# Optimization experiments

Hardware: AMD Instinct MI355X
Metric: run time of the kernel (lower is better)

## Reference

```python
import jax, jax.numpy as jnp
import numpy as np

B, S, D, H = 2, 2048, 1024, 16
HD = D // H  # head_dim = 64


def setup_inputs() -> dict:
    key = jax.random.key(0)
    k1, k2, k3 = jax.random.split(key, 3)
    x = jax.random.normal(k1, (B, S, D), dtype=jnp.float32)
    W_qkv = jax.random.normal(k2, (D, 3 * D), dtype=jnp.float32) * (D ** -0.5)
    b_qkv = jnp.zeros((3 * D,), dtype=jnp.float32)
    W_proj = jax.random.normal(k3, (D, D), dtype=jnp.float32) * (D ** -0.5)
    b_proj = jnp.zeros((D,), dtype=jnp.float32)
    return {"x": x, "W_qkv": W_qkv, "b_qkv": b_qkv, "W_proj": W_proj, "b_proj": b_proj}


def reference(x, W_qkv, b_qkv, W_proj, b_proj):
    b, s, d = x.shape
    scale = HD ** -0.5
    qkv = x @ W_qkv + b_qkv                       # [B,S,3D]
    q, k, v = jnp.split(qkv, 3, axis=-1)
    # [B,S,D] -> [B,H,S,HD]
    def to_heads(t):
        return t.reshape(b, s, H, HD).transpose(0, 2, 1, 3)
    q, k, v = map(to_heads, (q, k, v))
    scores = jnp.einsum('bhqd,bhkd->bhqk', q, k) * scale  # [B,H,S,S]
    causal = jnp.triu(jnp.ones((s, s), dtype=bool), k=1)
    scores = jnp.where(causal[None, None], -jnp.inf, scores)
    attn = jax.nn.softmax(scores, axis=-1)
    out = jnp.einsum('bhqk,bhkd->bhqd', attn, v)  # [B,H,S,HD]
    out = out.transpose(0, 2, 1, 3).reshape(b, s, d)
    return out @ W_proj + b_proj
```

## Files before the change

### kernel.cpp

```cpp
#include <hip/hip_runtime.h>

using frag_t = __attribute__((ext_vector_type(8))) short;
using f32x4  = __attribute__((ext_vector_type(4))) float;

#define L2E 1.4426950408889634f

#if __has_builtin(__builtin_amdgcn_exp2f)
#define EXP2(x) __builtin_amdgcn_exp2f(x)
#else
#define EXP2(x) exp2f(x)
#endif

constexpr int B_  = 2, S_ = 2048, D_ = 1024, H_ = 16, HD_ = 64;
constexpr int M_  = B_ * S_;
constexpr float QSCALE = 0.125f * L2E;

__device__ __forceinline__ ushort f2bf(float f) {
  union { float f; unsigned u; } v; v.f = f;
  unsigned u = v.u;
  unsigned r = (u + 0x7FFFu + ((u >> 16) & 1u)) >> 16;
  return (ushort)r;
}

__device__ __forceinline__ void gld_lds16(const ushort* g, ushort* l) {
  __builtin_amdgcn_global_load_lds((const __attribute__((address_space(1))) void*)g,
                                   (__attribute__((address_space(3))) void*)l, 16, 0, 0);
}

__global__ __launch_bounds__(256) void k_prep(
    const float* __restrict__ x, const float* __restrict__ Wqkv,
    const float* __restrict__ Wproj,
    ushort* __restrict__ Xbf, ushort* __restrict__ Wqt, ushort* __restrict__ Wpt) {
  int blk = blockIdx.x, tid = threadIdx.x;
  if (blk < 1024) {
    size_t base = (size_t)blk * 4096 + tid * 4;
    #pragma unroll
    for (int i = 0; i < 4; ++i) {
      float4 f = *(const float4*)(x + base + i * 1024);
      ushort4 o;
      o.x = f2bf(f.x); o.y = f2bf(f.y); o.z = f2bf(f.z); o.w = f2bf(f.w);
      *(ushort4*)(Xbf + base + i * 1024) = o;
    }
  } else {
    __shared__ float tile[64][65];
    const float* in; ushort* out; int N, K, bx, by;
    if (blk < 1024 + 768) { int b2 = blk - 1024; in = Wqkv;  out = Wqt; N = 3072; K = 1024; bx = b2 % 48; by = b2 / 48; }
    else                  { int b2 = blk - 1792; in = Wproj; out = Wpt; N = 1024; K = 1024; bx = b2 % 16; by = b2 / 16; }
    int n0 = bx * 64, k0 = by * 64;
    int tx = tid & 63, ty = tid >> 6;
    #pragma unroll
    for (int i = 0; i < 16; ++i)
      tile[ty + i * 4][tx] = in[(size_t)(k0 + ty + i * 4) * N + n0 + tx];
    __syncthreads();
    #pragma unroll
    for (int i = 0; i < 16; ++i)
      out[(size_t)(n0 + ty + i * 4) * K + k0 + tx] = f2bf(tile[tx][ty + i * 4]);
  }
}

__global__ __launch_bounds__(512, 2) void k_gemm8(
    const ushort* __restrict__ A, const ushort* __restrict__ Bt,
    const float* __restrict__ bias,
    ushort* __restrict__ Qo, ushort* __restrict__ Ko, ushort* __restrict__ Vo) {
  __shared__ ushort smem[65536];
  int tid = threadIdx.x;
  int lane = tid & 63, wave = tid >> 6;
  int quad = lane >> 4, li = lane & 15;
  int wm = wave >> 2, wn = wave & 3;
  int wg = blockIdx.x;
  int swz = (wg & 7) * 24 + (wg >> 3);
  int by = swz / 12, bx = swz % 12;
  int m0 = by * 256, n0 = bx * 256;
  const ushort* Asrc = A  + (size_t)m0 * 1024;
  const ushort* Bsrc = Bt + (size_t)n0 * 1024;
  int srow   = lane >> 2;
  int schunk = (lane & 3) ^ ((lane >> 4) & 3);
  int pos    = (quad ^ ((li >> 2) & 3)) * 8;

#define STG(BI, ISB, KS, KT) do { \
    const ushort* _s = (ISB) ? Bsrc : Asrc; \
    ushort* _d = &smem[((BI)*4 + (ISB)*2 + (KS)) * 8192]; \
    _Pragma("unroll") \
    for (int j = 0; j < 2; ++j) \
      gld_lds16(&_s[(size_t)(j*128 + wave*16 + srow) * 1024 + (KT)*64 + (KS)*32 + schunk*8], \
                &_d[(j*128 + wave*16) * 32]); \
  } while (0)

  f32x4 acc[8][4] = {};
  frag_t af[8], bf[2];

#define PH(BI, KS, NH, STGS, W4) do { \
    if ((NH) == 0) { \
      _Pragma("unroll") \
      for (int mi = 0; mi < 8; ++mi) \
        af[mi] = *(const frag_t*)&smem[((BI)*4 + (KS)) * 8192 + (wm*128 + mi*16 + li) * 32 + pos]; \
    } \
    _Pragma("unroll") \
    for (int nj = 0; nj < 2; ++nj) \
      bf[nj] = *(const frag_t*)&smem[((BI)*4 + 2 + (KS)) * 8192 + (wn*64 + ((NH)*2 + nj)*16 + li) * 32 + pos]; \
    STGS; \
    if (W4) asm volatile("s_waitcnt vmcnt(4)" ::: "memory"); \
    asm volatile("s_barrier" ::: "memory"); \
    __builtin_amdgcn_s_setprio(1); \
    _Pragma("unroll") \
    for (int mi = 0; mi < 8; ++mi) { \
      acc[mi][(NH)*2+0] = __builtin_amdgcn_mfma_f32_16x16x32_bf16(af[mi], bf[0], acc[mi][(NH)*2+0], 0, 0, 0); \
      acc[mi][(NH)*2+1] = __builtin_amdgcn_mfma_f32_16x16x32_bf16(af[mi], bf[1], acc[mi][(NH)*2+1], 0, 0, 0); \
    } \
    __builtin_amdgcn_s_setprio(0); \
    asm volatile("s_barrier" ::: "memory"); \
  } while (0)

  STG(0,0,0,0); STG(0,1,0,0); STG(0,0,1,0); STG(0,1,1,0);
  STG(1,0,0,1); STG(1,1,0,1);
  asm volatile("s_waitcnt vmcnt(4)" ::: "memory");
  asm volatile("s_barrier" ::: "memory");

  for (int it = 0; it < 8; ++it) {
    int t1 = 2*it + 1;
    int t2 = (2*it + 2 < 16) ? 2*it + 2 : 15;
    int t3 = (2*it + 3 < 16) ? 2*it + 3 : 15;
    PH(0,0,0, STG(1,0,1,t1), 0);
    PH(0,0,1, STG(1,1,1,t1), 0);
    PH(0,1,0, STG(0,0,0,t2), 0);
    PH(0,1,1, STG(0,1,0,t2), 1);
    PH(1,0,0, STG(0,0,1,t2), 0);
    PH(1,0,1, STG(0,1,1,t2), 0);
    PH(1,1,0, STG(1,0,0,t3), 0);
    PH(1,1,1, STG(1,1,0,t3), 1);
  }
#undef PH
#undef STG

  asm volatile("s_waitcnt vmcnt(0)" ::: "memory");
  __syncthreads();

  int which = (n0 + wn * 64) >> 10;
  if (which < 2) {
    #pragma unroll
    for (int ni = 0; ni < 4; ++ni) {
      int gcol = n0 + wn * 64 + ni * 16 + li;
      float bv = bias[gcol];
      int d = gcol & 1023, h = d >> 6, hd = d & 63;
      #pragma unroll
      for (int mi = 0; mi < 8; ++mi)
        #pragma unroll
        for (int r = 0; r < 4; ++r) {
          int grow = m0 + wm * 128 + mi * 16 + quad * 4 + r;
          int b = grow >> 11, s = grow & 2047;
          size_t off = (((size_t)b * H_ + h) * S_ + s) * HD_ + hd;
          float v = acc[mi][ni][r] + bv;
          if (which == 0) Qo[off] = f2bf(v * QSCALE);
          else            Ko[off] = f2bf(v);
        }
    }
  } else {
    ushort* vl = &smem[wave * 8192];
    #pragma unroll
    for (int ni = 0; ni < 4; ++ni) {
      int row = ni * 16 + li;
      float bv = bias[n0 + wn * 64 + row];
      int rx = (row & 7) << 3;
      #pragma unroll
      for (int mi = 0; mi < 8; ++mi) {
        int g  = (mi & 1) * 4 + quad;
        int gm = g & 3;
        int gp = (gm == 1 || gm == 2) ? (g ^ 3) : g;
        #pragma unroll
        for (int r = 0; r < 4; ++r) {
          int col = (mi >> 1) * 32 + gp * 4 + r;
          vl[row * 128 + (col ^ rx)] = f2bf(acc[mi][ni][r] + bv);
        }
      }
    }
    int h  = ((n0 & 1023) + wn * 64) >> 6;
    int b  = m0 >> 11;
    int s0 = (m0 & 2047) + wm * 128;
    size_t vbase = ((size_t)b * H_ + h) * HD_ * S_;
    #pragma unroll
    for (int i = 0; i < 16; ++i) {
      int row = i * 4 + quad;
      int col = li * 8;
      *(uint4*)&Vo[vbase + (size_t)row * S_ + s0 + col] =
          *(const uint4*)&vl[row * 128 + (col ^ ((row & 7) << 3))];
    }
  }
}

__global__ __launch_bounds__(256) void k_proj(
    const ushort* __restrict__ A, const ushort* __restrict__ Bt,
    const float* __restrict__ bias, float* __restrict__ Co) {
  constexpr int BM = 128, BN = 64, BK = 64, MI = 4, NI = 2;
  constexpr int N = 1024, K = 1024;
  __shared__ ushort smem[(BM + BN) * BK];
  ushort* As = smem;
  ushort* Bs = smem + BM * BK;
  int tid  = threadIdx.x;
  int lane = tid & 63, wave = tid >> 6;
  int quad = lane >> 4, li = lane & 15;
  int mbase = (wave >> 1) * (MI * 16);
  int nbase = (wave & 1) * 32;
  int m0 = blockIdx.y * BM, n0 = blockIdx.x * BN;
  int srow = lane >> 3;
  int scol = ((lane & 7) ^ srow) * 8;
  f32x4 acc[MI][NI] = {};
  for (int k0 = 0; k0 < K; k0 += BK) {
    #pragma unroll
    for (int i = 0; i < 4; ++i) {
      int rbase = i * 32 + wave * 8;
      gld_lds16(&A[(size_t)(m0 + rbase + srow) * K + k0 + scol], &As[rbase * BK]);
    }
    #pragma unroll
    for (int i = 0; i < 2; ++i) {
      int rbase = wave * 16 + i * 8;
      gld_lds16(&Bt[(size_t)(n0 + rbase + srow) * K + k0 + scol], &Bs[rbase * BK]);
    }
    __syncthreads();
    #pragma unroll
    for (int ks = 0; ks < 2; ++ks) {
      frag_t af[MI], bf[NI];
      #pragma unroll
      for (int mi = 0; mi < MI; ++mi)
        af[mi] = *(const frag_t*)&As[(mbase + mi * 16 + li) * BK + (((ks * 4 + quad) ^ (li & 7)) * 8)];
      #pragma unroll
      for (int ni = 0; ni < NI; ++ni)
        bf[ni] = *(const frag_t*)&Bs[(nbase + ni * 16 + li) * BK + (((ks * 4 + quad) ^ (li & 7)) * 8)];
      #pragma unroll
      for (int mi = 0; mi < MI; ++mi)
        #pragma unroll
        for (int ni = 0; ni < NI; ++ni)
          acc[mi][ni] = __builtin_amdgcn_mfma_f32_16x16x32_bf16(af[mi], bf[ni], acc[mi][ni], 0, 0, 0);
    }
    __syncthreads();
  }
  #pragma unroll
  for (int mi = 0; mi < MI; ++mi)
    #pragma unroll
    for (int ni = 0; ni < NI; ++ni) {
      int gcol = n0 + nbase + ni * 16 + li;
      float bv = bias[gcol];
      #pragma unroll
      for (int r = 0; r < 4; ++r) {
        int grow = m0 + mbase + mi * 16 + quad * 4 + r;
        Co[(size_t)grow * N + gcol] = acc[mi][ni][r] + bv;
      }
    }
}

__global__ __launch_bounds__(256) void k_attn(
    const ushort* __restrict__ Q, const ushort* __restrict__ K,
    const ushort* __restrict__ Vt, ushort* __restrict__ O) {
  __shared__ ushort Kbuf[2][64 * 64];
  __shared__ ushort Vbuf[2][64 * 64];
  int lane = threadIdx.x & 63, wave = threadIdx.x >> 6;
  int quad = lane >> 4, li = lane & 15;
  int bh = blockIdx.x;
  int yi = (int)blockIdx.y;
  int qb = (yi < 8) ? 31 - yi : (yi < 16) ? yi - 8 : (yi < 24) ? 39 - yi : yi - 16;
  int b = bh >> 4, hh = bh & 15;
  int q0 = qb * 64 + wave * 16;
  const ushort* Qb = Q  + (size_t)bh * S_ * HD_;
  const ushort* Kb = K  + (size_t)bh * S_ * HD_;
  const ushort* Vb = Vt + (size_t)bh * HD_ * S_;

  frag_t qf[2];
  #pragma unroll
  for (int ks = 0; ks < 2; ++ks)
    qf[ks] = *(const frag_t*)&Qb[(size_t)(q0 + li) * HD_ + ks * 32 + quad * 8];

  frag_t ones;
  #pragma unroll
  for (int i = 0; i < 8; ++i) ones[i] = (short)0x3F80;

  f32x4 o[4] = {};
  f32x4 lacc = {};

  auto stage = [&](int kb, int bi) {
    #pragma unroll
    for (int i = 0; i < 2; ++i) {
      int rt  = wave * 16 + i * 8 + (lane >> 3);
      int c16 = (lane & 7) ^ (lane >> 3);
      gld_lds16(&Kb[(size_t)(kb * 64 + rt) * HD_ + c16 * 8], &Kbuf[bi][(wave * 16 + i * 8) * 64]);
      gld_lds16(&Vb[(size_t)rt * S_ + kb * 64 + c16 * 8],    &Vbuf[bi][(wave * 16 + i * 8) * 64]);
    }
  };

  auto comp = [&](int kb, bool diag, int bi) {
    f32x4 sc[4];
    #pragma unroll
    for (int t = 0; t < 4; ++t) {
      f32x4 a = {};
      #pragma unroll
      for (int ks = 0; ks < 2; ++ks) {
        frag_t kf = *(const frag_t*)&Kbuf[bi][(t * 16 + li) * 64 + (((quad + ks * 4) ^ (li & 7)) * 8)];
        a = __builtin_amdgcn_mfma_f32_16x16x32_bf16(kf, qf[ks], a, 0, 0, 0);
      }
      sc[t] = a;
    }
    if (diag) {
      #pragma unroll
      for (int t = 0; t < 4; ++t) {
        int key = kb * 64 + t * 16 + quad * 4;
        #pragma unroll
        for (int r = 0; r < 4; ++r)
          if (key + r > q0 + li) sc[t][r] = -1e30f;
      }
    }
    #pragma unroll
    for (int t = 0; t < 4; ++t)
      #pragma unroll
      for (int r = 0; r < 4; ++r)
        sc[t][r] = EXP2(sc[t][r]);

    frag_t pf[2];
    #pragma unroll
    for (int ks = 0; ks < 2; ++ks) {
      unsigned w0e, w1e, w0o, w1o;
      asm("v_cvt_pk_bf16_f32 %0, %1, %2" : "=v"(w0e) : "v"(sc[2*ks][0]),   "v"(sc[2*ks][1]));
      asm("v_cvt_pk_bf16_f32 %0, %1, %2" : "=v"(w1e) : "v"(sc[2*ks][2]),   "v"(sc[2*ks][3]));
      asm("v_cvt_pk_bf16_f32 %0, %1, %2" : "=v"(w0o) : "v"(sc[2*ks+1][0]), "v"(sc[2*ks+1][1]));
      asm("v_cvt_pk_bf16_f32 %0, %1, %2" : "=v"(w1o) : "v"(sc[2*ks+1][2]), "v"(sc[2*ks+1][3]));
      asm("v_permlane32_swap_b32 %0, %1" : "+v"(w0e), "+v"(w0o));
      asm("v_permlane32_swap_b32 %0, %1" : "+v"(w1e), "+v"(w1o));
      union { frag_t f; unsigned u[4]; } pu;
      pu.u[0] = w0e; pu.u[1] = w1e; pu.u[2] = w0o; pu.u[3] = w1o;
      pf[ks] = pu.f;
    }
    lacc = __builtin_amdgcn_mfma_f32_16x16x32_bf16(ones, pf[0], lacc, 0, 0, 0);
    lacc = __builtin_amdgcn_mfma_f32_16x16x32_bf16(ones, pf[1], lacc, 0, 0, 0);
    #pragma unroll
    for (int ht = 0; ht < 4; ++ht)
      #pragma unroll
      for (int ks = 0; ks < 2; ++ks) {
        frag_t vtf = *(const frag_t*)&Vbuf[bi][(ht * 16 + li) * 64 + (((ks * 4 + quad) ^ (li & 7)) * 8)];
        o[ht] = __builtin_amdgcn_mfma_f32_16x16x32_bf16(vtf, pf[ks], o[ht], 0, 0, 0);
      }
  };

  stage(0, 0);
  __syncthreads();
  for (int kb = 0; kb <= qb; ++kb) {
    if (kb < qb) stage(kb + 1, (kb + 1) & 1);
    comp(kb, kb == qb, kb & 1);
    __syncthreads();
  }

  float inv = 1.f / lacc[0];
  int srow = q0 + li;
  size_t obase = ((size_t)b * S_ + srow) * D_ + hh * 64 + quad * 4;
  #pragma unroll
  for (int ht = 0; ht < 4; ++ht) {
    unsigned lo, hi;
    asm("v_cvt_pk_bf16_f32 %0, %1, %2" : "=v"(lo) : "v"(o[ht][0] * inv), "v"(o[ht][1] * inv));
    asm("v_cvt_pk_bf16_f32 %0, %1, %2" : "=v"(hi) : "v"(o[ht][2] * inv), "v"(o[ht][3] * inv));
    uint2 w; w.x = lo; w.y = hi;
    *(uint2*)&O[obase + ht * 16] = w;
  }
}

extern "C" void kernel_launch(void* const* d_in, const int* in_sizes, int n_in,
                              void* d_out, int out_size, void* d_ws, size_t ws_size,
                              hipStream_t stream) {
  (void)in_sizes; (void)n_in; (void)out_size; (void)ws_size;
  const float* x     = (const float*)d_in[0];
  const float* Wqkv  = (const float*)d_in[1];
  const float* bqkv  = (const float*)d_in[2];
  const float* Wproj = (const float*)d_in[3];
  const float* bproj = (const float*)d_in[4];
  float* out = (float*)d_out;

  char* ws = (char*)d_ws;
  ushort* Xbf = (ushort*)(ws);
  ushort* Wqt = (ushort*)(ws + (8u  << 20));
  ushort* Wpt = (ushort*)(ws + (14u << 20));
  ushort* Qbf = (ushort*)(ws + (16u << 20));
  ushort* Kbf = (ushort*)(ws + (24u << 20));
  ushort* Vtb = (ushort*)(ws + (32u << 20));
  ushort* Obf = Xbf;

  k_prep<<<dim3(2048), dim3(256), 0, stream>>>(x, Wqkv, Wproj, Xbf, Wqt, Wpt);
  k_gemm8<<<dim3(192), dim3(512), 0, stream>>>(Xbf, Wqt, bqkv, Qbf, Kbf, Vtb);
  k_attn<<<dim3(B_ * H_, 32), dim3(256), 0, stream>>>(Qbf, Kbf, Vtb, Obf);
  k_proj<<<dim3(16, 32), dim3(256), 0, stream>>>(Obf, Wpt, bproj, out);
}
```

Before: 168.4 us.

## Retile QKV GEMM to 128x384 blocks so the grid fills 256 workgroups

Changes the QKV projection GEMM from 256x256 tiles (192 workgroups) to 128x384 tiles (256 workgroups), which matches the CU count better and avoids a partial second wave. Wave layout becomes 4x2, with each wave computing 32x192, and the LDS staging and epilogue are reworked to suit. The V transpose epilogue now uses a small per-wave LDS buffer for each 16-column fragment. Arithmetic intensity per tile drops (128x384 versus 256x256), so more global and LDS traffic goes to A and B loads, and the B fragment register footprint grows.

```diff
diff --git a/kernel.cpp b/kernel.cpp
--- a/kernel.cpp
+++ b/kernel.cpp
@@ -66,53 +66,53 @@
   int tid = threadIdx.x;
   int lane = tid & 63, wave = tid >> 6;
   int quad = lane >> 4, li = lane & 15;
-  int wm = wave >> 2, wn = wave & 3;
+  int wm = wave >> 1, wn = wave & 1;
   int wg = blockIdx.x;
-  int swz = (wg & 7) * 24 + (wg >> 3);
-  int by = swz / 12, bx = swz % 12;
-  int m0 = by * 256, n0 = bx * 256;
+  int bx = wg & 7, by = wg >> 3;
+  int m0 = by * 128, n0 = bx * 384;
   const ushort* Asrc = A  + (size_t)m0 * 1024;
   const ushort* Bsrc = Bt + (size_t)n0 * 1024;
-  int srow   = lane >> 2;
-  int schunk = (lane & 3) ^ ((lane >> 4) & 3);
+  int schunk = (tid & 3) ^ ((tid >> 4) & 3);
   int pos    = (quad ^ ((li >> 2) & 3)) * 8;
 
-#define STG(BI, ISB, KS, KT) do { \
-    const ushort* _s = (ISB) ? Bsrc : Asrc; \
-    ushort* _d = &smem[((BI)*4 + (ISB)*2 + (KS)) * 8192]; \
+#define STGA(BI, KS, KT) \
+    gld_lds16(&Asrc[(size_t)(tid >> 2) * 1024 + (KT)*64 + (KS)*32 + schunk*8], \
+              &smem[(BI)*32768 + (KS)*4096 + wave*512])
+
+#define STGB(BI, KS, KT) do { \
     _Pragma("unroll") \
-    for (int j = 0; j < 2; ++j) \
-      gld_lds16(&_s[(size_t)(j*128 + wave*16 + srow) * 1024 + (KT)*64 + (KS)*32 + schunk*8], \
-                &_d[(j*128 + wave*16) * 32]); \
+    for (int p = 0; p < 3; ++p) \
+      gld_lds16(&Bsrc[(size_t)(p*128 + (tid >> 2)) * 1024 + (KT)*64 + (KS)*32 + schunk*8], \
+                &smem[(BI)*32768 + 8192 + (KS)*12288 + p*4096 + wave*512]); \
   } while (0)
 
-  f32x4 acc[8][4] = {};
-  frag_t af[8], bf[2];
+  f32x4 acc[2][12] = {};
+  frag_t af[2], bf[6];
 
 #define PH(BI, KS, NH, STGS, W4) do { \
     if ((NH) == 0) { \
       _Pragma("unroll") \
-      for (int mi = 0; mi < 8; ++mi) \
-        af[mi] = *(const frag_t*)&smem[((BI)*4 + (KS)) * 8192 + (wm*128 + mi*16 + li) * 32 + pos]; \
+      for (int mi = 0; mi < 2; ++mi) \
+        af[mi] = *(const frag_t*)&smem[(BI)*32768 + (KS)*4096 + (wm*32 + mi*16 + li)*32 + pos]; \
     } \
     _Pragma("unroll") \
-    for (int nj = 0; nj < 2; ++nj) \
-      bf[nj] = *(const frag_t*)&smem[((BI)*4 + 2 + (KS)) * 8192 + (wn*64 + ((NH)*2 + nj)*16 + li) * 32 + pos]; \
+    for (int nj = 0; nj < 6; ++nj) \
+      bf[nj] = *(const frag_t*)&smem[(BI)*32768 + 8192 + (KS)*12288 + (wn*192 + ((NH)*6 + nj)*16 + li)*32 + pos]; \
     STGS; \
     if (W4) asm volatile("s_waitcnt vmcnt(4)" ::: "memory"); \
     asm volatile("s_barrier" ::: "memory"); \
     __builtin_amdgcn_s_setprio(1); \
     _Pragma("unroll") \
-    for (int mi = 0; mi < 8; ++mi) { \
-      acc[mi][(NH)*2+0] = __builtin_amdgcn_mfma_f32_16x16x32_bf16(af[mi], bf[0], acc[mi][(NH)*2+0], 0, 0, 0); \
-      acc[mi][(NH)*2+1] = __builtin_amdgcn_mfma_f32_16x16x32_bf16(af[mi], bf[1], acc[mi][(NH)*2+1], 0, 0, 0); \
-    } \
+    for (int mi = 0; mi < 2; ++mi) \
+      _Pragma("unroll") \
+      for (int nj = 0; nj < 6; ++nj) \
+        acc[mi][(NH)*6 + nj] = __builtin_amdgcn_mfma_f32_16x16x32_bf16(af[mi], bf[nj], acc[mi][(NH)*6 + nj], 0, 0, 0); \
     __builtin_amdgcn_s_setprio(0); \
     asm volatile("s_barrier" ::: "memory"); \
   } while (0)
 
-  STG(0,0,0,0); STG(0,1,0,0); STG(0,0,1,0); STG(0,1,1,0);
-  STG(1,0,0,1); STG(1,1,0,1);
+  STGA(0,0,0); STGB(0,0,0); STGA(0,1,0); STGB(0,1,0);
+  STGA(1,0,1); STGB(1,0,1);
   asm volatile("s_waitcnt vmcnt(4)" ::: "memory");
   asm volatile("s_barrier" ::: "memory");
 
@@ -120,69 +120,56 @@
     int t1 = 2*it + 1;
     int t2 = (2*it + 2 < 16) ? 2*it + 2 : 15;
     int t3 = (2*it + 3 < 16) ? 2*it + 3 : 15;
-    PH(0,0,0, STG(1,0,1,t1), 0);
-    PH(0,0,1, STG(1,1,1,t1), 0);
-    PH(0,1,0, STG(0,0,0,t2), 0);
-    PH(0,1,1, STG(0,1,0,t2), 1);
-    PH(1,0,0, STG(0,0,1,t2), 0);
-    PH(1,0,1, STG(0,1,1,t2), 0);
-    PH(1,1,0, STG(1,0,0,t3), 0);
-    PH(1,1,1, STG(1,1,0,t3), 1);
+    PH(0,0,0, STGA(1,1,t1), 0);
+    PH(0,0,1, STGB(1,1,t1), 0);
+    PH(0,1,0, STGA(0,0,t2), 0);
+    PH(0,1,1, STGB(0,0,t2), 1);
+    PH(1,0,0, STGA(0,1,t2), 0);
+    PH(1,0,1, STGB(0,1,t2), 0);
+    PH(1,1,0, STGA(1,0,t3), 0);
+    PH(1,1,1, STGB(1,0,t3), 1);
   }
 #undef PH
-#undef STG
+#undef STGA
+#undef STGB
 
   asm volatile("s_waitcnt vmcnt(0)" ::: "memory");
   __syncthreads();
 
-  int which = (n0 + wn * 64) >> 10;
-  if (which < 2) {
-    #pragma unroll
-    for (int ni = 0; ni < 4; ++ni) {
-      int gcol = n0 + wn * 64 + ni * 16 + li;
-      float bv = bias[gcol];
-      int d = gcol & 1023, h = d >> 6, hd = d & 63;
-      #pragma unroll
-      for (int mi = 0; mi < 8; ++mi)
+  #pragma unroll
+  for (int nf = 0; nf < 12; ++nf) {
+    int col0 = n0 + wn * 192 + nf * 16;
+    int which = col0 >> 10;
+    float bv = bias[col0 + li];
+    if (which < 2) {
+      int d = (col0 + li) & 1023;
+      int h = d >> 6, hd = d & 63;
+      #pragma unroll
+      for (int mi = 0; mi < 2; ++mi)
         #pragma unroll
         for (int r = 0; r < 4; ++r) {
-          int grow = m0 + wm * 128 + mi * 16 + quad * 4 + r;
+          int grow = m0 + wm * 32 + mi * 16 + quad * 4 + r;
           int b = grow >> 11, s = grow & 2047;
           size_t off = (((size_t)b * H_ + h) * S_ + s) * HD_ + hd;
-          float v = acc[mi][ni][r] + bv;
+          float v = acc[mi][nf][r] + bv;
           if (which == 0) Qo[off] = f2bf(v * QSCALE);
           else            Ko[off] = f2bf(v);
         }
-    }
-  } else {
-    ushort* vl = &smem[wave * 8192];
-    #pragma unroll
-    for (int ni = 0; ni < 4; ++ni) {
-      int row = ni * 16 + li;
-      float bv = bias[n0 + wn * 64 + row];
-      int rx = (row & 7) << 3;
-      #pragma unroll
-      for (int mi = 0; mi < 8; ++mi) {
-        int g  = (mi & 1) * 4 + quad;
-        int gm = g & 3;
-        int gp = (gm == 1 || gm == 2) ? (g ^ 3) : g;
+    } else {
+      ushort* vl = &smem[wave * 640];
+      int gq = (quad == 1 || quad == 2) ? (quad ^ 3) : quad;
+      #pragma unroll
+      for (int mi = 0; mi < 2; ++mi) {
+        union { ushort u[4]; uint2 w; } pk;
         #pragma unroll
-        for (int r = 0; r < 4; ++r) {
-          int col = (mi >> 1) * 32 + gp * 4 + r;
-          vl[row * 128 + (col ^ rx)] = f2bf(acc[mi][ni][r] + bv);
-        }
-      }
-    }
-    int h  = ((n0 & 1023) + wn * 64) >> 6;
-    int b  = m0 >> 11;
-    int s0 = (m0 & 2047) + wm * 128;
-    size_t vbase = ((size_t)b * H_ + h) * HD_ * S_;
-    #pragma unroll
-    for (int i = 0; i < 16; ++i) {
-      int row = i * 4 + quad;
-      int col = li * 8;
-      *(uint4*)&Vo[vbase + (size_t)row * S_ + s0 + col] =
-          *(const uint4*)&vl[row * 128 + (col ^ ((row & 7) << 3))];
+        for (int r = 0; r < 4; ++r) pk.u[r] = f2bf(acc[mi][nf][r] + bv);
+        *(uint2*)&vl[li * 40 + mi * 16 + gq * 4] = pk.w;
+      }
+      int h = (col0 >> 6) & 15, hd0 = col0 & 63;
+      int b = m0 >> 11, s0 = (m0 & 2047) + wm * 32;
+      int rt = lane >> 2, kc = (lane & 3) * 8;
+      uint4 w = *(const uint4*)&vl[rt * 40 + kc];
+      *(uint4*)&Vo[((size_t)(b * H_ + h) * HD_ + hd0 + rt) * S_ + s0 + kc] = w;
     }
   }
 }
@@ -379,7 +366,7 @@
   ushort* Obf = Xbf;
 
   k_prep<<<dim3(2048), dim3(256), 0, stream>>>(x, Wqkv, Wproj, Xbf, Wqt, Wpt);
-  k_gemm8<<<dim3(192), dim3(512), 0, stream>>>(Xbf, Wqt, bqkv, Qbf, Kbf, Vtb);
+  k_gemm8<<<dim3(256), dim3(512), 0, stream>>>(Xbf, Wqt, bqkv, Qbf, Kbf, Vtb);
   k_attn<<<dim3(B_ * H_, 32), dim3(256), 0, stream>>>(Qbf, Kbf, Vtb, Obf);
   k_proj<<<dim3(16, 32), dim3(256), 0, stream>>>(Obf, Wpt, bproj, out);
 }
```

Result: no change. 165.8 us (-1.5%).

## Replace 256x256 pipelined QKV GEMM with simpler 128x128 single-buffered kernel

Applied to the files above, without the earlier changes.

Replaces the heavily software-pipelined 256x256-tile, 512-thread QKV GEMM (double-buffered LDS, manual vmcnt waits, setprio) with a 128x128-tile, 256-thread kernel that loads each K-slice and synchronizes before computing. The grid grows from 192 to 768 blocks, which should fill more CUs and allow more resident blocks per CU. The V-transpose epilogue is also rewritten to stage 16-row chunks through a small per-wave LDS buffer. The cost is less operand reuse per tile and no overlap between global loads and MFMA inside a block.

```diff
diff --git a/kernel.cpp b/kernel.cpp
--- a/kernel.cpp
+++ b/kernel.cpp
@@ -12,7 +12,6 @@
 #endif
 
 constexpr int B_  = 2, S_ = 2048, D_ = 1024, H_ = 16, HD_ = 64;
-constexpr int M_  = B_ * S_;
 constexpr float QSCALE = 0.125f * L2E;
 
 __device__ __forceinline__ ushort f2bf(float f) {
@@ -58,95 +57,66 @@
   }
 }
 
-__global__ __launch_bounds__(512, 2) void k_gemm8(
+__global__ __launch_bounds__(256) void k_qkv(
     const ushort* __restrict__ A, const ushort* __restrict__ Bt,
     const float* __restrict__ bias,
     ushort* __restrict__ Qo, ushort* __restrict__ Ko, ushort* __restrict__ Vo) {
-  __shared__ ushort smem[65536];
-  int tid = threadIdx.x;
+  constexpr int BM = 128, BN = 128, BK = 64, MI = 4, NI = 4;
+  constexpr int K = 1024;
+  __shared__ ushort smem[(BM + BN) * BK];
+  ushort* As = smem;
+  ushort* Bs = smem + BM * BK;
+  int tid  = threadIdx.x;
   int lane = tid & 63, wave = tid >> 6;
   int quad = lane >> 4, li = lane & 15;
-  int wm = wave >> 2, wn = wave & 3;
-  int wg = blockIdx.x;
-  int swz = (wg & 7) * 24 + (wg >> 3);
-  int by = swz / 12, bx = swz % 12;
-  int m0 = by * 256, n0 = bx * 256;
-  const ushort* Asrc = A  + (size_t)m0 * 1024;
-  const ushort* Bsrc = Bt + (size_t)n0 * 1024;
-  int srow   = lane >> 2;
-  int schunk = (lane & 3) ^ ((lane >> 4) & 3);
-  int pos    = (quad ^ ((li >> 2) & 3)) * 8;
-
-#define STG(BI, ISB, KS, KT) do { \
-    const ushort* _s = (ISB) ? Bsrc : Asrc; \
-    ushort* _d = &smem[((BI)*4 + (ISB)*2 + (KS)) * 8192]; \
-    _Pragma("unroll") \
-    for (int j = 0; j < 2; ++j) \
-      gld_lds16(&_s[(size_t)(j*128 + wave*16 + srow) * 1024 + (KT)*64 + (KS)*32 + schunk*8], \
-                &_d[(j*128 + wave*16) * 32]); \
-  } while (0)
-
-  f32x4 acc[8][4] = {};
-  frag_t af[8], bf[2];
-
-#define PH(BI, KS, NH, STGS, W4) do { \
-    if ((NH) == 0) { \
-      _Pragma("unroll") \
-      for (int mi = 0; mi < 8; ++mi) \
-        af[mi] = *(const frag_t*)&smem[((BI)*4 + (KS)) * 8192 + (wm*128 + mi*16 + li) * 32 + pos]; \
-    } \
-    _Pragma("unroll") \
-    for (int nj = 0; nj < 2; ++nj) \
-      bf[nj] = *(const frag_t*)&smem[((BI)*4 + 2 + (KS)) * 8192 + (wn*64 + ((NH)*2 + nj)*16 + li) * 32 + pos]; \
-    STGS; \
-    if (W4) asm volatile("s_waitcnt vmcnt(4)" ::: "memory"); \
-    asm volatile("s_barrier" ::: "memory"); \
-    __builtin_amdgcn_s_setprio(1); \
-    _Pragma("unroll") \
-    for (int mi = 0; mi < 8; ++mi) { \
-      acc[mi][(NH)*2+0] = __builtin_amdgcn_mfma_f32_16x16x32_bf16(af[mi], bf[0], acc[mi][(NH)*2+0], 0, 0, 0); \
-      acc[mi][(NH)*2+1] = __builtin_amdgcn_mfma_f32_16x16x32_bf16(af[mi], bf[1], acc[mi][(NH)*2+1], 0, 0, 0); \
-    } \
-    __builtin_amdgcn_s_setprio(0); \
-    asm volatile("s_barrier" ::: "memory"); \
-  } while (0)
-
-  STG(0,0,0,0); STG(0,1,0,0); STG(0,0,1,0); STG(0,1,1,0);
-  STG(1,0,0,1); STG(1,1,0,1);
-  asm volatile("s_waitcnt vmcnt(4)" ::: "memory");
-  asm volatile("s_barrier" ::: "memory");
-
-  for (int it = 0; it < 8; ++it) {
-    int t1 = 2*it + 1;
-    int t2 = (2*it + 2 < 16) ? 2*it + 2 : 15;
-    int t3 = (2*it + 3 < 16) ? 2*it + 3 : 15;
-    PH(0,0,0, STG(1,0,1,t1), 0);
-    PH(0,0,1, STG(1,1,1,t1), 0);
-    PH(0,1,0, STG(0,0,0,t2), 0);
-    PH(0,1,1, STG(0,1,0,t2), 1);
-    PH(1,0,0, STG(0,0,1,t2), 0);
-    PH(1,0,1, STG(0,1,1,t2), 0);
-    PH(1,1,0, STG(1,0,0,t3), 0);
-    PH(1,1,1, STG(1,1,0,t3), 1);
-  }
-#undef PH
-#undef STG
-
-  asm volatile("s_waitcnt vmcnt(0)" ::: "memory");
-  __syncthreads();
-
-  int which = (n0 + wn * 64) >> 10;
+  int mbase = (wave >> 1) * 64;
+  int nbase = (wave & 1) * 64;
+  int m0 = blockIdx.y * BM, n0 = blockIdx.x * BN;
+  int srow = lane >> 3;
+  int scol = ((lane & 7) ^ srow) * 8;
+  f32x4 acc[MI][NI] = {};
+  for (int k0 = 0; k0 < K; k0 += BK) {
+    #pragma unroll
+    for (int i = 0; i < 4; ++i) {
+      int rbase = i * 32 + wave * 8;
+      gld_lds16(&A[(size_t)(m0 + rbase + srow) * K + k0 + scol], &As[rbase * BK]);
+    }
+    #pragma unroll
+    for (int i = 0; i < 4; ++i) {
+      int rbase = i * 32 + wave * 8;
+      gld_lds16(&Bt[(size_t)(n0 + rbase + srow) * K + k0 + scol], &Bs[rbase * BK]);
+    }
+    __syncthreads();
+    #pragma unroll
+    for (int ks = 0; ks < 2; ++ks) {
+      frag_t af[MI], bf[NI];
+      #pragma unroll
+      for (int mi = 0; mi < MI; ++mi)
+        af[mi] = *(const frag_t*)&As[(mbase + mi * 16 + li) * BK + (((ks * 4 + quad) ^ (li & 7)) * 8)];
+      #pragma unroll
+      for (int ni = 0; ni < NI; ++ni)
+        bf[ni] = *(const frag_t*)&Bs[(nbase + ni * 16 + li) * BK + (((ks * 4 + quad) ^ (li & 7)) * 8)];
+      #pragma unroll
+      for (int mi = 0; mi < MI; ++mi)
+        #pragma unroll
+        for (int ni = 0; ni < NI; ++ni)
+          acc[mi][ni] = __builtin_amdgcn_mfma_f32_16x16x32_bf16(af[mi], bf[ni], acc[mi][ni], 0, 0, 0);
+    }
+    __syncthreads();
+  }
+  int col0 = n0 + nbase;
+  int which = col0 >> 10;
   if (which < 2) {
     #pragma unroll
-    for (int ni = 0; ni < 4; ++ni) {
-      int gcol = n0 + wn * 64 + ni * 16 + li;
+    for (int ni = 0; ni < NI; ++ni) {
+      int gcol = col0 + ni * 16 + li;
       float bv = bias[gcol];
       int d = gcol & 1023, h = d >> 6, hd = d & 63;
       #pragma unroll
-      for (int mi = 0; mi < 8; ++mi)
+      for (int mi = 0; mi < MI; ++mi)
         #pragma unroll
         for (int r = 0; r < 4; ++r) {
-          int grow = m0 + wm * 128 + mi * 16 + quad * 4 + r;
+          int grow = m0 + mbase + mi * 16 + quad * 4 + r;
           int b = grow >> 11, s = grow & 2047;
           size_t off = (((size_t)b * H_ + h) * S_ + s) * HD_ + hd;
           float v = acc[mi][ni][r] + bv;
@@ -155,34 +125,30 @@
         }
     }
   } else {
-    ushort* vl = &smem[wave * 8192];
-    #pragma unroll
-    for (int ni = 0; ni < 4; ++ni) {
-      int row = ni * 16 + li;
-      float bv = bias[n0 + wn * 64 + row];
-      int rx = (row & 7) << 3;
-      #pragma unroll
-      for (int mi = 0; mi < 8; ++mi) {
+    ushort* vl = smem + wave * 1152;
+    int h  = (col0 >> 6) & 15;
+    int b  = m0 >> 11, s0 = (m0 & 2047) + mbase;
+    size_t vbase = (size_t)(b * H_ + h) * HD_ * S_;
+    #pragma unroll
+    for (int ni = 0; ni < NI; ++ni) {
+      float bv = bias[col0 + ni * 16 + li];
+      #pragma unroll
+      for (int mi = 0; mi < MI; ++mi) {
         int g  = (mi & 1) * 4 + quad;
         int gm = g & 3;
         int gp = (gm == 1 || gm == 2) ? (g ^ 3) : g;
-        #pragma unroll
-        for (int r = 0; r < 4; ++r) {
-          int col = (mi >> 1) * 32 + gp * 4 + r;
-          vl[row * 128 + (col ^ rx)] = f2bf(acc[mi][ni][r] + bv);
-        }
-      }
-    }
-    int h  = ((n0 & 1023) + wn * 64) >> 6;
-    int b  = m0 >> 11;
-    int s0 = (m0 & 2047) + wm * 128;
-    size_t vbase = ((size_t)b * H_ + h) * HD_ * S_;
-    #pragma unroll
-    for (int i = 0; i < 16; ++i) {
-      int row = i * 4 + quad;
-      int col = li * 8;
-      *(uint4*)&Vo[vbase + (size_t)row * S_ + s0 + col] =
-          *(const uint4*)&vl[row * 128 + (col ^ ((row & 7) << 3))];
+        union { ushort u[4]; uint2 w; } pk;
+        #pragma unroll
+        for (int r = 0; r < 4; ++r) pk.u[r] = f2bf(acc[mi][ni][r] + bv);
+        *(uint2*)&vl[li * 72 + (mi >> 1) * 32 + gp * 4] = pk.w;
+      }
+      #pragma unroll
+      for (int i = 0; i < 2; ++i) {
+        int slot = i * 64 + lane;
+        int row = slot >> 3, kc = (slot & 7) * 8;
+        uint4 w = *(const uint4*)&vl[row * 72 + kc];
+        *(uint4*)&Vo[vbase + (size_t)(ni * 16 + row) * S_ + s0 + kc] = w;
+      }
     }
   }
 }
@@ -379,7 +345,7 @@
   ushort* Obf = Xbf;
 
   k_prep<<<dim3(2048), dim3(256), 0, stream>>>(x, Wqkv, Wproj, Xbf, Wqt, Wpt);
-  k_gemm8<<<dim3(192), dim3(512), 0, stream>>>(Xbf, Wqt, bqkv, Qbf, Kbf, Vtb);
+  k_qkv<<<dim3(24, 32), dim3(256), 0, stream>>>(Xbf, Wqt, bqkv, Qbf, Kbf, Vtb);
   k_attn<<<dim3(B_ * H_, 32), dim3(256), 0, stream>>>(Qbf, Kbf, Vtb, Obf);
   k_proj<<<dim3(16, 32), dim3(256), 0, stream>>>(Obf, Wpt, bproj, out);
 }
```

Result: slower. 174.1 us (+3.4%).
